# Performance work log

Measured on AMD Instinct MI355X. Metric: run time of the kernel, lower is better.

## Reference

```python
import jax, jax.numpy as jnp
import numpy as np

D_MSA = 256
D_PAIR = 128
N_HEADS = 8
HEAD_DIM = D_MSA // N_HEADS
EPS = 1e-5


def setup_inputs() -> dict:
    key = jax.random.key(0)
    ks = jax.random.split(key, 14)
    s = 0.02
    return {
        "msa": jax.random.normal(ks[0], (1, 64, 256, D_MSA), dtype=jnp.float32),
        "pair": jax.random.normal(ks[1], (1, 256, 256, D_PAIR), dtype=jnp.float32),
        "Wq": jax.random.normal(ks[2], (D_MSA, D_MSA), dtype=jnp.float32) * s,
        "bq": jnp.zeros((D_MSA,), jnp.float32),
        "Wk": jax.random.normal(ks[3], (D_MSA, D_MSA), dtype=jnp.float32) * s,
        "bk": jnp.zeros((D_MSA,), jnp.float32),
        "Wv": jax.random.normal(ks[4], (D_MSA, D_MSA), dtype=jnp.float32) * s,
        "bv": jnp.zeros((D_MSA,), jnp.float32),
        "Wpb": jax.random.normal(ks[5], (D_PAIR, N_HEADS), dtype=jnp.float32) * s,
        "bpb": jnp.zeros((N_HEADS,), jnp.float32),
        "Wo": jax.random.normal(ks[6], (D_MSA, D_MSA), dtype=jnp.float32) * s,
        "bo": jnp.zeros((D_MSA,), jnp.float32),
        "gamma": jnp.ones((D_MSA,), jnp.float32),
        "beta": jnp.zeros((D_MSA,), jnp.float32),
    }


def reference(msa, pair, Wq, bq, Wk, bk, Wv, bv, Wpb, bpb, Wo, bo, gamma, beta):
    B, N, L, D = msa.shape
    H, Hd = N_HEADS, HEAD_DIM
    # projections -> (B, N, L, H, Hd)
    q = (msa @ Wq + bq).reshape(B, N, L, H, Hd)
    k = (msa @ Wk + bk).reshape(B, N, L, H, Hd)
    v = (msa @ Wv + bv).reshape(B, N, L, H, Hd)
    # scores: (B, N, H, L, L)
    scores = jnp.einsum('bnihd,bnjhd->bnhij', q, k) / jnp.sqrt(jnp.float32(Hd))
    # pair bias: (B, L, L, H) -> (B, H, L, L), broadcast over N
    pb = jnp.transpose(pair @ Wpb + bpb, (0, 3, 1, 2))
    scores = scores + pb[:, None]
    attn = jax.nn.softmax(scores, axis=-1)
    attn_out = jnp.einsum('bnhij,bnjhd->bnihd', attn, v).reshape(B, N, L, D)
    attn_out = attn_out @ Wo + bo
    # residual + LayerNorm
    x = msa + attn_out
    mu = jnp.mean(x, axis=-1, keepdims=True)
    var = jnp.var(x, axis=-1, keepdims=True)
    return (x - mu) * jax.lax.rsqrt(var + EPS) * gamma + beta
```

## Files before the change

kernel.cpp:

```cpp
#include <hip/hip_runtime.h>

#define NSEQ 64
#define LL   256
#define DD   256
#define HH   8
#define HDIM 32

typedef short short8  __attribute__((ext_vector_type(8)));
typedef short short4v __attribute__((ext_vector_type(4)));
typedef float float4v __attribute__((ext_vector_type(4)));

#define MFMA16(a,b,c) __builtin_amdgcn_mfma_f32_16x16x32_bf16((a),(b),(c),0,0,0)

__device__ __forceinline__ float4v zero4() {
  float4v z;
  z[0] = 0.f; z[1] = 0.f; z[2] = 0.f; z[3] = 0.f;
  return z;
}

__device__ __forceinline__ short f2b(float f) {
  unsigned u = __float_as_uint(f);
  u = (u + 0x7fffu + ((u >> 16) & 1u)) >> 16;
  return (short)u;
}

__device__ __forceinline__ float b2f(short s) {
  return __uint_as_float(((unsigned)(unsigned short)s) << 16);
}

__device__ __forceinline__ unsigned pkbf(float a, float b) {
  unsigned r;
  asm volatile("v_cvt_pk_bf16_f32 %0, %1, %2" : "=v"(r) : "v"(a), "v"(b));
  return r;
}

__device__ __forceinline__ void ld_lds16(const void* g, void* l) {
  __builtin_amdgcn_global_load_lds(
      (const __attribute__((address_space(1))) unsigned int*)g,
      (__attribute__((address_space(3))) unsigned int*)l, 16, 0, 0);
}
#define WAIT_VM0() __builtin_amdgcn_s_waitcnt(0x0F70)

#define WT_OFF    0
#define PB_OFF    (4*65536*2)
#define PBF_OFF   (PB_OFF + 8*65536*2)
#define Q_OFF     (PB_OFF + 8*65536*4)
#define K_OFF     (Q_OFF  + 16384*256*2)
#define VT_OFF    (K_OFF  + 16384*256*2)
#define MSA16_OFF (VT_OFF + 16384*256*2)
#define O_OFF     MSA16_OFF

__global__ __launch_bounds__(256) void k1_prep(
    const float* __restrict__ msa,  const float* __restrict__ pair,
    const float* __restrict__ Wq,   const float* __restrict__ Wk,
    const float* __restrict__ Wv,   const float* __restrict__ Wpb,
    const float* __restrict__ bpb,  const float* __restrict__ Wo,
    char* __restrict__ ws)
{
  __shared__ __align__(16) short shm[4 * 64 * 128];
  __shared__ short ldsWt[16 * 136];
  int bx = blockIdx.x, tid = threadIdx.x;
  if (bx < 256) {
    short* pb16 = (short*)(ws + PB_OFF);
    for (int i = tid; i < 16 * 136; i += 256) ldsWt[i] = 0;
    __syncthreads();
    {
      float4 wv4 = *(const float4*)&Wpb[tid * 4];
      int kk = (tid * 4) >> 3, n0 = (tid * 4) & 7;
      ldsWt[(n0 + 0) * 136 + kk] = f2b(wv4.x);
      ldsWt[(n0 + 1) * 136 + kk] = f2b(wv4.y);
      ldsWt[(n0 + 2) * 136 + kk] = f2b(wv4.z);
      ldsWt[(n0 + 3) * 136 + kk] = f2b(wv4.w);
    }
    __syncthreads();
    int w = tid >> 6, l = tid & 63, q = l >> 4, c = l & 15;
    int base = bx * 256 + w * 64;
    short* lsWw = shm + w * 8192;
#pragma unroll
    for (int it = 0; it < 16; it++) {
      int jl = it * 4 + (l >> 4);
      int kc = l & 15;
      const float* src = &pair[(base + jl) * 128 + kc * 8];
      float4 a = *(const float4*)src;
      float4 b = *(const float4*)(src + 4);
      short8 v8;
      v8[0] = f2b(a.x); v8[1] = f2b(a.y); v8[2] = f2b(a.z); v8[3] = f2b(a.w);
      v8[4] = f2b(b.x); v8[5] = f2b(b.y); v8[6] = f2b(b.z); v8[7] = f2b(b.w);
      *(short8*)&lsWw[jl * 128 + ((kc ^ (jl & 7)) * 8)] = v8;
    }
    float bias = bpb[c & 7];
    short8 bf[4];
#pragma unroll
    for (int ks = 0; ks < 4; ks++)
      bf[ks] = *(const short8*)&ldsWt[c * 136 + ks * 32 + q * 8];
    float4v acc[4];
#pragma unroll
    for (int mt = 0; mt < 4; mt++) acc[mt] = zero4();
#pragma unroll
    for (int ks = 0; ks < 4; ks++) {
#pragma unroll
      for (int mt = 0; mt < 4; mt++) {
        int row = mt * 16 + c;
        short8 af = *(const short8*)&lsWw[row * 128 + (((ks * 4 + q) ^ (c & 7)) * 8)];
        acc[mt] = MFMA16(af, bf[ks], acc[mt]);
      }
    }
    if (c < 8) {
#pragma unroll
      for (int mt = 0; mt < 4; mt++) {
        short4v o;
#pragma unroll
        for (int r = 0; r < 4; r++)
          o[r] = f2b((acc[mt][r] + bias) * 1.44269504088896f);
        *(short4v*)&pb16[c * 65536 + base + mt * 16 + q * 4] = o;
      }
    }
  } else if (bx < 320) {
    int b2 = bx - 256;
    int mat = b2 >> 4, sub = b2 & 15;
    int k0 = (sub >> 2) * 64, n0 = (sub & 3) * 64;
    const float* W = (mat == 0) ? Wq : (mat == 1) ? Wk : (mat == 2) ? Wv : Wo;
    short* wt = (short*)(ws + WT_OFF) + mat * 65536;
    short* ldsT = shm;
#pragma unroll
    for (int p = 0; p < 4; p++) {
      int kl = p * 16 + (tid >> 4);
      int nl = (tid & 15) * 4;
      float4 v = *(const float4*)&W[(k0 + kl) * 256 + n0 + nl];
      ldsT[(nl + 0) * 72 + kl] = f2b(v.x);
      ldsT[(nl + 1) * 72 + kl] = f2b(v.y);
      ldsT[(nl + 2) * 72 + kl] = f2b(v.z);
      ldsT[(nl + 3) * 72 + kl] = f2b(v.w);
    }
    __syncthreads();
#pragma unroll
    for (int p = 0; p < 2; p++) {
      int id = p * 256 + tid;
      int nl = id >> 3, c8 = id & 7;
      *(short8*)&wt[(n0 + nl) * 256 + k0 + c8 * 8] =
          *(const short8*)&ldsT[nl * 72 + c8 * 8];
    }
  } else {
    int b3 = bx - 320;
    const float* src = msa + b3 * 8192;
    short* dst = (short*)(ws + MSA16_OFF) + b3 * 8192;
#pragma unroll
    for (int i = 0; i < 8; i++) {
      int idx = i * 1024 + tid * 4;
      float4 v = *(const float4*)&src[idx];
      short4v s;
      s[0] = f2b(v.x); s[1] = f2b(v.y); s[2] = f2b(v.z); s[3] = f2b(v.w);
      *(short4v*)&dst[idx] = s;
    }
  }
}

__global__ __launch_bounds__(256) void k2_qkv(
    const float* __restrict__ bq, const float* __restrict__ bk,
    const float* __restrict__ bv, char* __restrict__ ws)
{
  __shared__ __align__(16) short ls[2 * 128 * 128];
  short* lsA = ls;
  short* lsB = ls + 16384;
  int bx = blockIdx.x, tid = threadIdx.x;
  if (bx >= 768) {
    int b = bx - 768;
    int it16 = b & 15;
    const short* src = (const short*)(ws + PB_OFF) + (b >> 4) * 65536 + it16 * 4096;
    short* pbf = (short*)(ws + PBF_OFF);
    short* lt = lsA;
#pragma unroll
    for (int i2 = 0; i2 < 2; i2++) {
      int idx = i2 * 2048 + tid * 8;
      *(short8*)&lt[(idx >> 8) * 264 + (idx & 255)] = *(const short8*)&src[idx];
    }
    __syncthreads();
#pragma unroll
    for (int i2 = 0; i2 < 4; i2++) {
      int fid = i2 * 256 + tid;
      int jt = fid >> 6, lane = fid & 63;
      int qp = lane >> 4, cp = lane & 15;
      short4v v = *(const short4v*)&lt[cp * 264 + jt * 16 + qp * 4];
      *(short4v*)&pbf[((b * 16 + jt) * 64 + lane) * 4] = v;
    }
    return;
  }
  int rt = bx & 127, ct = bx >> 7;
  int m = ct >> 1, cb = (ct & 1) * 128;
  int R0 = rt * 128;
  const short* msa16 = (const short*)(ws + MSA16_OFF);
  const short* wt = (const short*)(ws + WT_OFF) + m * 65536;
  int w = tid >> 6, l = tid & 63, q = l >> 4, c = l & 15;
  int WR = (w & 1) * 64, WC = (w >> 1) * 64;
  float4v acc[4][4];
#pragma unroll
  for (int mt = 0; mt < 4; mt++)
#pragma unroll
    for (int nt = 0; nt < 4; nt++) acc[mt][nt] = zero4();

#pragma unroll 1
  for (int kk = 0; kk < 2; kk++) {
    if (kk) __syncthreads();
#pragma unroll
    for (int i = 0; i < 8; i++) {
      int ci = i * 256 + tid;
      int r = ci >> 4, pos = ci & 15;
      int kc = pos ^ (r & 7);
      ld_lds16(&msa16[(R0 + r) * 256 + kk * 128 + kc * 8], &lsA[ci * 8]);
    }
#pragma unroll
    for (int i = 0; i < 8; i++) {
      int ci = i * 256 + tid;
      int r = ci >> 4, pos = ci & 15;
      int kc = pos ^ (r & 7);
      ld_lds16(&wt[(cb + r) * 256 + kk * 128 + kc * 8], &lsB[ci * 8]);
    }
    WAIT_VM0();
    __syncthreads();
#pragma unroll
    for (int ks = 0; ks < 4; ks++) {
      short8 af[4], bf[4];
#pragma unroll
      for (int mt = 0; mt < 4; mt++) {
        int r = WR + mt * 16 + c;
        int phys = (ks * 4 + q) ^ (r & 7);
        af[mt] = *(const short8*)&lsA[r * 128 + phys * 8];
      }
#pragma unroll
      for (int nt = 0; nt < 4; nt++) {
        int r = WC + nt * 16 + c;
        int phys = (ks * 4 + q) ^ (r & 7);
        bf[nt] = *(const short8*)&lsB[r * 128 + phys * 8];
      }
#pragma unroll
      for (int mt = 0; mt < 4; mt++)
#pragma unroll
        for (int nt = 0; nt < 4; nt++)
          acc[mt][nt] = MFMA16(af[mt], bf[nt], acc[mt][nt]);
    }
  }

  const float* bp = (m == 0) ? bq : (m == 1) ? bk : bv;
  int n = R0 >> 8;
  __syncthreads();
  short* lsC = ls;
  if (m < 2) {
#pragma unroll
    for (int nt = 0; nt < 4; nt++) {
      float bb = bp[cb + WC + nt * 16 + c];
#pragma unroll
      for (int mt = 0; mt < 4; mt++)
#pragma unroll
        for (int r = 0; r < 4; r++)
          lsC[(WR + mt * 16 + q * 4 + r) * 136 + WC + nt * 16 + c] =
              f2b(acc[mt][nt][r] + bb);
    }
    __syncthreads();
    short* dst = (short*)(ws + (m == 0 ? Q_OFF : K_OFF)) + n * 65536;
    int ibase = R0 & 255;
#pragma unroll
    for (int p = 0; p < 8; p++) {
      int id = p * 256 + tid;
      int il = id >> 4, ch8 = id & 15;
      int chg = cb + ch8 * 8;
      int hh = chg >> 5, hd0 = chg & 31;
      *(short8*)&dst[(hh * 256 + ibase + il) * 32 + hd0] =
          *(const short8*)&lsC[il * 136 + ch8 * 8];
    }
  } else {
#pragma unroll
    for (int nt = 0; nt < 4; nt++) {
      float bb = bp[cb + WC + nt * 16 + c];
#pragma unroll
      for (int mt = 0; mt < 4; mt++)
#pragma unroll
        for (int r = 0; r < 4; r++)
          lsC[(WC + nt * 16 + c) * 136 + WR + mt * 16 + q * 4 + r] =
              f2b(acc[mt][nt][r] + bb);
    }
    __syncthreads();
    short* vt = (short*)(ws + VT_OFF) + n * 65536;
    int jbase = R0 & 255;
#pragma unroll
    for (int p = 0; p < 8; p++) {
      int id = p * 256 + tid;
      int chl = id >> 4, j8 = id & 15;
      int chg = cb + chl;
      *(short8*)&vt[chg * 256 + jbase + j8 * 8] =
          *(const short8*)&lsC[chl * 136 + j8 * 8];
    }
  }
}

__global__ __launch_bounds__(256, 4) void k3_attn(char* __restrict__ ws)
{
  __shared__ __align__(16) short lds[16896];
  short* lsK = lds;
  short* lsP = lds;
  short* lsV = lds + 8704;
  int bx = blockIdx.x, tid = threadIdx.x;
  int qq = bx >> 9, grp = bx & 511;
  int n = grp >> 3, h = grp & 7;
  int w = tid >> 6, l = tid & 63, q = l >> 4, c = l & 15;
  const short* qh = (const short*)(ws + Q_OFF) + (n * HH + h) * 256 * HDIM;
  const short* kh = (const short*)(ws + K_OFF) + (n * HH + h) * 256 * HDIM;
  const short* vt = (const short*)(ws + VT_OFF) + (n * HH + h) * HDIM * 256;
  const short* pbf = (const short*)(ws + PBF_OFF) + (h * 16 + qq * 4 + w) * 16 * 256;
  short* os = (short*)(ws + O_OFF);
  const float scl2 = 0.17677669529663687f * 1.44269504088896f;
  int i0 = qq * 64 + w * 16;

  short8 aq = *(const short8*)&qh[(i0 + c) * HDIM + q * 8];
  short4v pv[16];
#pragma unroll
  for (int jt = 0; jt < 16; jt++)
    pv[jt] = *(const short4v*)&pbf[(jt * 64 + l) * 4];

#pragma unroll
  for (int i = 0; i < 4; i++) {
    int ci = i * 256 + tid;
    ld_lds16(&kh[ci * 8], &lsK[ci * 8]);
  }
#pragma unroll
  for (int i = 0; i < 4; i++) {
    int ci = i * 256 + tid;
    int row = ci >> 5, j = ci & 31;
    int sj = j ^ (row & 7);
    ld_lds16(&vt[row * 256 + sj * 8], &lsV[ci * 8]);
  }
  WAIT_VM0();
  __syncthreads();

  float4v s[16];
#pragma unroll
  for (int jt = 0; jt < 16; jt++) {
    short8 kf = *(const short8*)&lsK[(jt * 16 + c) * 32 + q * 8];
    s[jt] = MFMA16(kf, aq, zero4());
  }
#pragma unroll
  for (int jt = 0; jt < 16; jt++) {
#pragma unroll
    for (int r = 0; r < 4; r++)
      s[jt][r] = __builtin_fmaf(s[jt][r], scl2, b2f(pv[jt][r]));
  }
  float t[16];
#pragma unroll
  for (int jt = 0; jt < 16; jt++)
    t[jt] = fmaxf(fmaxf(s[jt][0], s[jt][1]), fmaxf(s[jt][2], s[jt][3]));
#pragma unroll
  for (int st = 8; st >= 1; st >>= 1)
#pragma unroll
    for (int i = 0; i < st; i++) t[i] = fmaxf(t[i], t[i + st]);
  float m = fmaxf(t[0], __shfl_xor(t[0], 16, 64));
  m = fmaxf(m, __shfl_xor(m, 32, 64));
#pragma unroll
  for (int jt = 0; jt < 16; jt++) {
#pragma unroll
    for (int r = 0; r < 4; r++) s[jt][r] = exp2f(s[jt][r] - m);
    t[jt] = (s[jt][0] + s[jt][1]) + (s[jt][2] + s[jt][3]);
  }
#pragma unroll
  for (int st = 8; st >= 1; st >>= 1)
#pragma unroll
    for (int i = 0; i < st; i++) t[i] += t[i + st];
  float rs = t[0];
  rs += __shfl_xor(rs, 16, 64);
  rs += __shfl_xor(rs, 32, 64);
  float inv = 1.f / rs;

  __syncthreads();

  int pw = w * 2176 + c * 136;
  float4v o0 = zero4(), o1 = zero4();
#pragma unroll
  for (int ch = 0; ch < 2; ch++) {
#pragma unroll
    for (int jt2 = 0; jt2 < 8; jt2++) {
      int jt = ch * 8 + jt2;
      uint2 u;
      u.x = pkbf(s[jt][0], s[jt][1]);
      u.y = pkbf(s[jt][2], s[jt][3]);
      *(uint2*)&lsP[pw + jt2 * 16 + q * 4] = u;
    }
#pragma unroll
    for (int kk2 = 0; kk2 < 4; kk2++) {
      int kk = ch * 4 + kk2;
      short8 pf = *(const short8*)&lsP[pw + kk2 * 32 + q * 8];
      int sl0 = ((kk * 4 + q) ^ (c & 7)) * 8;
      short8 b0 = *(const short8*)&lsV[c * 256 + sl0];
      short8 b1 = *(const short8*)&lsV[(16 + c) * 256 + sl0];
      o0 = MFMA16(b0, pf, o0);
      o1 = MFMA16(b1, pf, o1);
    }
  }
  short* orow = &os[(n * 256 + i0 + c) * 256 + h * 32];
  short4v t0, t1;
#pragma unroll
  for (int r = 0; r < 4; r++) {
    t0[r] = f2b(o0[r] * inv);
    t1[r] = f2b(o1[r] * inv);
  }
  *(short4v*)&orow[q * 4] = t0;
  *(short4v*)&orow[16 + q * 4] = t1;
}

__global__ __launch_bounds__(256) void k4_out(
    const float* __restrict__ msa, const float* __restrict__ bo,
    const float* __restrict__ gamma, const float* __restrict__ beta,
    const char* __restrict__ ws, float* __restrict__ out)
{
  __shared__ __align__(16) short lsA[32 * 128];
  __shared__ __align__(16) short lsB[256 * 128];
  __shared__ float sred[2][32][2];
  int bx = blockIdx.x, tid = threadIdx.x;
  int w = tid >> 6, l = tid & 63, q = l >> 4, c = l & 15;
  int rg = w >> 1, ch2 = w & 1;
  int R0 = bx * 32;
  int Rw = R0 + rg * 16;
  int C0 = ch2 * 128;
  const short* osrc = (const short*)(ws + O_OFF);
  const short* wto  = (const short*)(ws + WT_OFF) + 3 * 65536;

  float4v acc[8];
#pragma unroll
  for (int nt = 0; nt < 8; nt++) acc[nt] = zero4();

#pragma unroll 1
  for (int kk = 0; kk < 2; kk++) {
    if (kk) __syncthreads();
#pragma unroll
    for (int i = 0; i < 2; i++) {
      int ci = i * 256 + tid;
      int r = ci >> 4, pos = ci & 15;
      int kc = pos ^ (r & 7);
      ld_lds16(&osrc[(R0 + r) * 256 + kk * 128 + kc * 8], &lsA[ci * 8]);
    }
#pragma unroll
    for (int i = 0; i < 16; i++) {
      int ci = i * 256 + tid;
      int r = ci >> 4, pos = ci & 15;
      int kc = pos ^ (r & 7);
      ld_lds16(&wto[r * 256 + kk * 128 + kc * 8], &lsB[ci * 8]);
    }
    WAIT_VM0();
    __syncthreads();
#pragma unroll
    for (int ks = 0; ks < 4; ks++) {
      int rA = rg * 16 + c;
      int physA = (ks * 4 + q) ^ (rA & 7);
      short8 af = *(const short8*)&lsA[rA * 128 + physA * 8];
#pragma unroll
      for (int nt = 0; nt < 8; nt++) {
        int rB = C0 + nt * 16 + c;
        int phys = (ks * 4 + q) ^ (rB & 7);
        short8 bf = *(const short8*)&lsB[rB * 128 + phys * 8];
        acc[nt] = MFMA16(af, bf, acc[nt]);
      }
    }
  }

  float s1[4] = {0, 0, 0, 0}, s2[4] = {0, 0, 0, 0};
#pragma unroll
  for (int nt = 0; nt < 8; nt++) {
    float bb = bo[C0 + nt * 16 + c];
#pragma unroll
    for (int r = 0; r < 4; r++) {
      float x = acc[nt][r] + bb + msa[(Rw + q * 4 + r) * 256 + C0 + nt * 16 + c];
      acc[nt][r] = x;
      s1[r] += x;
      s2[r] = __builtin_fmaf(x, x, s2[r]);
    }
  }
#pragma unroll
  for (int r = 0; r < 4; r++) {
    s1[r] += __shfl_xor(s1[r], 1, 64); s2[r] += __shfl_xor(s2[r], 1, 64);
    s1[r] += __shfl_xor(s1[r], 2, 64); s2[r] += __shfl_xor(s2[r], 2, 64);
    s1[r] += __shfl_xor(s1[r], 4, 64); s2[r] += __shfl_xor(s2[r], 4, 64);
    s1[r] += __shfl_xor(s1[r], 8, 64); s2[r] += __shfl_xor(s2[r], 8, 64);
  }
  if (c == 0) {
#pragma unroll
    for (int r = 0; r < 4; r++) {
      sred[0][rg * 16 + q * 4 + r][ch2] = s1[r];
      sred[1][rg * 16 + q * 4 + r][ch2] = s2[r];
    }
  }
  __syncthreads();
  float mu[4], rsd[4];
#pragma unroll
  for (int r = 0; r < 4; r++) {
    int row = rg * 16 + q * 4 + r;
    float a = sred[0][row][0] + sred[0][row][1];
    float b = sred[1][row][0] + sred[1][row][1];
    float m = a * (1.f / 256.f);
    float v = __builtin_fmaf(-m, m, b * (1.f / 256.f));
    mu[r] = m;
    rsd[r] = rsqrtf(v + 1e-5f);
  }
#pragma unroll
  for (int nt = 0; nt < 8; nt++) {
    float g = gamma[nt * 16 + c + C0], bt = beta[nt * 16 + c + C0];
#pragma unroll
    for (int r = 0; r < 4; r++)
      out[(Rw + q * 4 + r) * 256 + C0 + nt * 16 + c] =
          (acc[nt][r] - mu[r]) * rsd[r] * g + bt;
  }
}

extern "C" void kernel_launch(void* const* d_in, const int* in_sizes, int n_in,
                              void* d_out, int out_size, void* d_ws, size_t ws_size,
                              hipStream_t stream)
{
  const float* msa   = (const float*)d_in[0];
  const float* pair  = (const float*)d_in[1];
  const float* Wq    = (const float*)d_in[2];
  const float* bq    = (const float*)d_in[3];
  const float* Wk    = (const float*)d_in[4];
  const float* bk    = (const float*)d_in[5];
  const float* Wv    = (const float*)d_in[6];
  const float* bv    = (const float*)d_in[7];
  const float* Wpb   = (const float*)d_in[8];
  const float* bpb   = (const float*)d_in[9];
  const float* Wo    = (const float*)d_in[10];
  const float* bo    = (const float*)d_in[11];
  const float* gamma = (const float*)d_in[12];
  const float* beta  = (const float*)d_in[13];
  char* ws = (char*)d_ws;
  float* out = (float*)d_out;

  hipLaunchKernelGGL(k1_prep, dim3(832), dim3(256), 0, stream,
                     msa, pair, Wq, Wk, Wv, Wpb, bpb, Wo, ws);
  hipLaunchKernelGGL(k2_qkv, dim3(896), dim3(256), 0, stream,
                     bq, bk, bv, ws);
  hipLaunchKernelGGL(k3_attn, dim3(2048), dim3(256), 0, stream, ws);
  hipLaunchKernelGGL(k4_out, dim3(512), dim3(256), 0, stream,
                     msa, bo, gamma, beta, ws, out);
}
```

Before: 156.3 us.

## Merge attention blocks per (seq, head) to reuse K/V tiles across all queries

The attention kernel now launches one 512-thread block per (sequence, head) instead of four 256-thread blocks. Each wave processes two 16-row query tiles in a loop, so K and V for a head are loaded into LDS once instead of four times. The P staging buffer gets its own LDS region instead of aliasing K. A partial vmcnt wait lets the first QK^T MFMA start once K has landed while V is still loading. The cost is fewer blocks (512) and a larger LDS footprint per block, which may lower occupancy. Work per wave is also serialized over two query tiles.

```diff
diff --git a/kernel.cpp b/kernel.cpp
--- a/kernel.cpp
+++ b/kernel.cpp
@@ -40,6 +40,7 @@
       (__attribute__((address_space(3))) unsigned int*)l, 16, 0, 0);
 }
 #define WAIT_VM0() __builtin_amdgcn_s_waitcnt(0x0F70)
+#define WAIT_VM2() __builtin_amdgcn_s_waitcnt(0x0F72)
 
 #define WT_OFF    0
 #define PB_OFF    (4*65536*2)
@@ -292,116 +293,142 @@
   }
 }
 
-__global__ __launch_bounds__(256, 4) void k3_attn(char* __restrict__ ws)
+__global__ __launch_bounds__(512, 4) void k3_attn(char* __restrict__ ws)
 {
-  __shared__ __align__(16) short lds[16896];
+  __shared__ __align__(16) short lds[8192 + 8192 + 8 * 2176];
   short* lsK = lds;
-  short* lsP = lds;
-  short* lsV = lds + 8704;
+  short* lsV = lds + 8192;
+  short* lsP = lds + 16384;
   int bx = blockIdx.x, tid = threadIdx.x;
-  int qq = bx >> 9, grp = bx & 511;
-  int n = grp >> 3, h = grp & 7;
+  int n = bx >> 3, h = bx & 7;
   int w = tid >> 6, l = tid & 63, q = l >> 4, c = l & 15;
+  int w4 = w & 3, wh = w >> 2;
   const short* qh = (const short*)(ws + Q_OFF) + (n * HH + h) * 256 * HDIM;
   const short* kh = (const short*)(ws + K_OFF) + (n * HH + h) * 256 * HDIM;
   const short* vt = (const short*)(ws + VT_OFF) + (n * HH + h) * HDIM * 256;
-  const short* pbf = (const short*)(ws + PBF_OFF) + (h * 16 + qq * 4 + w) * 16 * 256;
+  const short* pbfh = (const short*)(ws + PBF_OFF) + h * 16 * 16 * 256;
   short* os = (short*)(ws + O_OFF);
   const float scl2 = 0.17677669529663687f * 1.44269504088896f;
-  int i0 = qq * 64 + w * 16;
-
-  short8 aq = *(const short8*)&qh[(i0 + c) * HDIM + q * 8];
-  short4v pv[16];
+
+  int qq0 = wh * 2;
+  int i00 = qq0 * 64 + w4 * 16;
+  int i01 = i00 + 128;
+  i01 = (qq0 + 1) * 64 + w4 * 16;
+
+  short8 aq0 = *(const short8*)&qh[(i00 + c) * HDIM + q * 8];
+  const short* pbf0 = pbfh + (qq0 * 4 + w4) * 16 * 256;
+  short4v pv0[16];
 #pragma unroll
   for (int jt = 0; jt < 16; jt++)
-    pv[jt] = *(const short4v*)&pbf[(jt * 64 + l) * 4];
-
-#pragma unroll
-  for (int i = 0; i < 4; i++) {
-    int ci = i * 256 + tid;
+    pv0[jt] = *(const short4v*)&pbf0[(jt * 64 + l) * 4];
+
+#pragma unroll
+  for (int i = 0; i < 2; i++) {
+    int ci = i * 512 + tid;
     ld_lds16(&kh[ci * 8], &lsK[ci * 8]);
   }
 #pragma unroll
-  for (int i = 0; i < 4; i++) {
-    int ci = i * 256 + tid;
+  for (int i = 0; i < 2; i++) {
+    int ci = i * 512 + tid;
     int row = ci >> 5, j = ci & 31;
     int sj = j ^ (row & 7);
     ld_lds16(&vt[row * 256 + sj * 8], &lsV[ci * 8]);
   }
+  WAIT_VM2();
+  __syncthreads();
+
+  int pw = w * 2176 + c * 136;
+  float4v s[16];
+  float t[16];
+
+#pragma unroll
+  for (int jt = 0; jt < 16; jt++) {
+    short8 kf = *(const short8*)&lsK[(jt * 16 + c) * 32 + q * 8];
+    s[jt] = MFMA16(kf, aq0, zero4());
+  }
   WAIT_VM0();
   __syncthreads();
 
-  float4v s[16];
-#pragma unroll
-  for (int jt = 0; jt < 16; jt++) {
-    short8 kf = *(const short8*)&lsK[(jt * 16 + c) * 32 + q * 8];
-    s[jt] = MFMA16(kf, aq, zero4());
-  }
-#pragma unroll
-  for (int jt = 0; jt < 16; jt++) {
-#pragma unroll
-    for (int r = 0; r < 4; r++)
-      s[jt][r] = __builtin_fmaf(s[jt][r], scl2, b2f(pv[jt][r]));
-  }
-  float t[16];
+  short8 aq1 = *(const short8*)&qh[(i01 + c) * HDIM + q * 8];
+  const short* pbf1 = pbfh + ((qq0 + 1) * 4 + w4) * 16 * 256;
+  short4v pv1[16];
 #pragma unroll
   for (int jt = 0; jt < 16; jt++)
-    t[jt] = fmaxf(fmaxf(s[jt][0], s[jt][1]), fmaxf(s[jt][2], s[jt][3]));
-#pragma unroll
-  for (int st = 8; st >= 1; st >>= 1)
-#pragma unroll
-    for (int i = 0; i < st; i++) t[i] = fmaxf(t[i], t[i + st]);
-  float m = fmaxf(t[0], __shfl_xor(t[0], 16, 64));
-  m = fmaxf(m, __shfl_xor(m, 32, 64));
-#pragma unroll
-  for (int jt = 0; jt < 16; jt++) {
-#pragma unroll
-    for (int r = 0; r < 4; r++) s[jt][r] = exp2f(s[jt][r] - m);
-    t[jt] = (s[jt][0] + s[jt][1]) + (s[jt][2] + s[jt][3]);
-  }
-#pragma unroll
-  for (int st = 8; st >= 1; st >>= 1)
-#pragma unroll
-    for (int i = 0; i < st; i++) t[i] += t[i + st];
-  float rs = t[0];
-  rs += __shfl_xor(rs, 16, 64);
-  rs += __shfl_xor(rs, 32, 64);
-  float inv = 1.f / rs;
-
-  __syncthreads();
-
-  int pw = w * 2176 + c * 136;
-  float4v o0 = zero4(), o1 = zero4();
-#pragma unroll
-  for (int ch = 0; ch < 2; ch++) {
-#pragma unroll
-    for (int jt2 = 0; jt2 < 8; jt2++) {
-      int jt = ch * 8 + jt2;
-      uint2 u;
-      u.x = pkbf(s[jt][0], s[jt][1]);
-      u.y = pkbf(s[jt][2], s[jt][3]);
-      *(uint2*)&lsP[pw + jt2 * 16 + q * 4] = u;
-    }
-#pragma unroll
-    for (int kk2 = 0; kk2 < 4; kk2++) {
-      int kk = ch * 4 + kk2;
-      short8 pf = *(const short8*)&lsP[pw + kk2 * 32 + q * 8];
-      int sl0 = ((kk * 4 + q) ^ (c & 7)) * 8;
-      short8 b0 = *(const short8*)&lsV[c * 256 + sl0];
-      short8 b1 = *(const short8*)&lsV[(16 + c) * 256 + sl0];
-      o0 = MFMA16(b0, pf, o0);
-      o1 = MFMA16(b1, pf, o1);
-    }
-  }
-  short* orow = &os[(n * 256 + i0 + c) * 256 + h * 32];
-  short4v t0, t1;
-#pragma unroll
-  for (int r = 0; r < 4; r++) {
-    t0[r] = f2b(o0[r] * inv);
-    t1[r] = f2b(o1[r] * inv);
-  }
-  *(short4v*)&orow[q * 4] = t0;
-  *(short4v*)&orow[16 + q * 4] = t1;
+    pv1[jt] = *(const short4v*)&pbf1[(jt * 64 + l) * 4];
+
+#pragma unroll 1
+  for (int tt = 0; tt < 2; tt++) {
+    int i0 = tt ? i01 : i00;
+    if (tt) {
+#pragma unroll
+      for (int jt = 0; jt < 16; jt++) {
+        short8 kf = *(const short8*)&lsK[(jt * 16 + c) * 32 + q * 8];
+        s[jt] = MFMA16(kf, aq1, zero4());
+      }
+    }
+#pragma unroll
+    for (int jt = 0; jt < 16; jt++) {
+      short4v pv = tt ? pv1[jt] : pv0[jt];
+#pragma unroll
+      for (int r = 0; r < 4; r++)
+        s[jt][r] = __builtin_fmaf(s[jt][r], scl2, b2f(pv[r]));
+    }
+#pragma unroll
+    for (int jt = 0; jt < 16; jt++)
+      t[jt] = fmaxf(fmaxf(s[jt][0], s[jt][1]), fmaxf(s[jt][2], s[jt][3]));
+#pragma unroll
+    for (int st = 8; st >= 1; st >>= 1)
+#pragma unroll
+      for (int i = 0; i < st; i++) t[i] = fmaxf(t[i], t[i + st]);
+    float m = fmaxf(t[0], __shfl_xor(t[0], 16, 64));
+    m = fmaxf(m, __shfl_xor(m, 32, 64));
+#pragma unroll
+    for (int jt = 0; jt < 16; jt++) {
+#pragma unroll
+      for (int r = 0; r < 4; r++) s[jt][r] = exp2f(s[jt][r] - m);
+      t[jt] = (s[jt][0] + s[jt][1]) + (s[jt][2] + s[jt][3]);
+    }
+#pragma unroll
+    for (int st = 8; st >= 1; st >>= 1)
+#pragma unroll
+      for (int i = 0; i < st; i++) t[i] += t[i + st];
+    float rs = t[0];
+    rs += __shfl_xor(rs, 16, 64);
+    rs += __shfl_xor(rs, 32, 64);
+    float inv = 1.f / rs;
+
+    float4v o0 = zero4(), o1 = zero4();
+#pragma unroll
+    for (int ch = 0; ch < 2; ch++) {
+#pragma unroll
+      for (int jt2 = 0; jt2 < 8; jt2++) {
+        int jt = ch * 8 + jt2;
+        uint2 u;
+        u.x = pkbf(s[jt][0], s[jt][1]);
+        u.y = pkbf(s[jt][2], s[jt][3]);
+        *(uint2*)&lsP[pw + jt2 * 16 + q * 4] = u;
+      }
+#pragma unroll
+      for (int kk2 = 0; kk2 < 4; kk2++) {
+        int kk = ch * 4 + kk2;
+        short8 pf = *(const short8*)&lsP[pw + kk2 * 32 + q * 8];
+        int sl0 = ((kk * 4 + q) ^ (c & 7)) * 8;
+        short8 b0 = *(const short8*)&lsV[c * 256 + sl0];
+        short8 b1 = *(const short8*)&lsV[(16 + c) * 256 + sl0];
+        o0 = MFMA16(b0, pf, o0);
+        o1 = MFMA16(b1, pf, o1);
+      }
+    }
+    short* orow = &os[(n * 256 + i0 + c) * 256 + h * 32];
+    short4v t0, t1;
+#pragma unroll
+    for (int r = 0; r < 4; r++) {
+      t0[r] = f2b(o0[r] * inv);
+      t1[r] = f2b(o1[r] * inv);
+    }
+    *(short4v*)&orow[q * 4] = t0;
+    *(short4v*)&orow[16 + q * 4] = t1;
+  }
 }
 
 __global__ __launch_bounds__(256) void k4_out(
@@ -532,7 +559,7 @@
                      msa, pair, Wq, Wk, Wv, Wpb, bpb, Wo, ws);
   hipLaunchKernelGGL(k2_qkv, dim3(896), dim3(256), 0, stream,
                      bq, bk, bv, ws);
-  hipLaunchKernelGGL(k3_attn, dim3(2048), dim3(256), 0, stream, ws);
+  hipLaunchKernelGGL(k3_attn, dim3(512), dim3(512), 0, stream, ws);
   hipLaunchKernelGGL(k4_out, dim3(512), dim3(256), 0, stream,
                      msa, bo, gamma, beta, ws, out);
 }
```

After: 185.6 us. +18.8%, slower.
